# Optimization experiments

Hardware: AMD Instinct MI355X
Metric: run time of the kernel (lower is better)

## Reference

```python
import jax, jax.numpy as jnp
import numpy as np

N_NODES = 100000
IN_CH = 128
OUT_CH = 128
N_EDGES = 1700000


def setup_inputs() -> dict:
    key = jax.random.key(0)
    k_x, k_e, k_w = jax.random.split(key, 3)
    x = jax.random.normal(k_x, (N_NODES, IN_CH), dtype=jnp.float32)
    # edges: one self-loop per node (guarantees deg>=1 for every node),
    # remainder random
    loops = jnp.stack([jnp.arange(N_NODES, dtype=jnp.int64)] * 2)  # [2, N]
    rand = jax.random.randint(k_e, (2, N_EDGES - N_NODES), 0, N_NODES, dtype=jnp.int64)
    edge_index = jnp.concatenate([loops, rand], axis=1)  # [2, E]
    # glorot-uniform weight, zero bias (reset_parameters)
    limit = float(np.sqrt(6.0 / (IN_CH + OUT_CH)))
    weight = jax.random.uniform(k_w, (IN_CH, OUT_CH), dtype=jnp.float32,
                                minval=-limit, maxval=limit)
    bias = jnp.zeros((OUT_CH,), dtype=jnp.float32)
    return {"x": x, "edge_index": edge_index, "weight": weight, "bias": bias}


def reference(x, edge_index, weight, bias):
    row, col = edge_index[0], edge_index[1]
    # deg = bincount(row) over all N nodes
    deg = jax.ops.segment_sum(jnp.ones_like(row, dtype=jnp.float32), row,
                              num_segments=x.shape[0])
    deg_inv_sqrt = deg ** -0.5  # symmetric normalization
    norm = deg_inv_sqrt[row] * deg_inv_sqrt[col]  # [E]
    support = x @ weight  # [N, out]
    msgs = norm[:, None] * support[col]  # [E, out] gather + scale
    out = jax.ops.segment_sum(msgs, row, num_segments=x.shape[0])  # scatter-add
    return out + bias
```

## Files before the change

### kernel.cpp

```cpp
#include <hip/hip_runtime.h>
#include <hip/hip_bf16.h>


#define NBLK_B 512
#define BSHIFT 7
#define NPB    128

typedef __attribute__((ext_vector_type(8))) short bf16x8;
typedef __attribute__((ext_vector_type(4))) float f32x4;

__device__ __forceinline__ uint32_t f2bf_rne(float f) {
    uint32_t u = __float_as_uint(f);
    return (u + 0x7fffu + ((u >> 16) & 1u)) >> 16;
}
__device__ __forceinline__ float bf_lo(uint32_t u) { return __uint_as_float(u << 16); }
__device__ __forceinline__ float bf_hi(uint32_t u) { return __uint_as_float(u & 0xffff0000u); }

__device__ __forceinline__ bf16x8 pack8(float4 lo, float4 hi) {
    union { bf16x8 v; ushort u[8]; } r;
    r.u[0] = (ushort)f2bf_rne(lo.x);
    r.u[1] = (ushort)f2bf_rne(lo.y);
    r.u[2] = (ushort)f2bf_rne(lo.z);
    r.u[3] = (ushort)f2bf_rne(lo.w);
    r.u[4] = (ushort)f2bf_rne(hi.x);
    r.u[5] = (ushort)f2bf_rne(hi.y);
    r.u[6] = (ushort)f2bf_rne(hi.z);
    r.u[7] = (ushort)f2bf_rne(hi.w);
    return r.v;
}

__global__ void wconv_kernel(const float* __restrict__ W, ushort* __restrict__ Wt,
                             int* __restrict__ gcur, int nbuck) {
    int t = blockIdx.x * blockDim.x + threadIdx.x;
    int n = t >> 7, k = t & 127;
    Wt[n * 128 + k] = (ushort)f2bf_rne(W[k * 128 + n]);
    if (t < nbuck) gcur[t] = 0;
}

__global__ __launch_bounds__(256) void merged_kernel(
        const float* __restrict__ X, const ushort* __restrict__ Wt,
        uint32_t* __restrict__ S, int N,
        const int* __restrict__ row, const int* __restrict__ col,
        uint32_t* __restrict__ part, int* __restrict__ gcur,
        int E, int chunk, int nbuck, int cap, int GB) {
    __shared__ int h[1024];
    if ((int)blockIdx.x < GB) {
        const int wave = threadIdx.x >> 6;
        const int lane = threadIdx.x & 63;
        const int c16  = lane & 15;
        const int kg   = lane >> 4;
        const int row0 = blockIdx.x * 128 + wave * 32;

        int rA0 = row0 + c16;
        int rA1 = row0 + 16 + c16;
        if (rA0 >= N) rA0 = N - 1;
        if (rA1 >= N) rA1 = N - 1;

        f32x4 acc[2][8];
#pragma unroll
        for (int m = 0; m < 2; ++m)
#pragma unroll
            for (int cb = 0; cb < 8; ++cb) acc[m][cb] = (f32x4){0.f, 0.f, 0.f, 0.f};

        const float*  xa0 = X + (size_t)rA0 * 128 + kg * 8;
        const float*  xa1 = X + (size_t)rA1 * 128 + kg * 8;
        const ushort* wb  = Wt + kg * 8 + c16 * 128;

#pragma unroll
        for (int kk = 0; kk < 4; ++kk) {
            float4 a0lo = *(const float4*)(xa0 + kk * 32);
            float4 a0hi = *(const float4*)(xa0 + kk * 32 + 4);
            float4 a1lo = *(const float4*)(xa1 + kk * 32);
            float4 a1hi = *(const float4*)(xa1 + kk * 32 + 4);
            bf16x8 A0 = pack8(a0lo, a0hi);
            bf16x8 A1 = pack8(a1lo, a1hi);
#pragma unroll
            for (int cb = 0; cb < 8; ++cb) {
                bf16x8 B = *(const bf16x8*)(wb + (size_t)cb * 16 * 128 + kk * 32);
                acc[0][cb] = __builtin_amdgcn_mfma_f32_16x16x32_bf16(A0, B, acc[0][cb], 0, 0, 0);
                acc[1][cb] = __builtin_amdgcn_mfma_f32_16x16x32_bf16(A1, B, acc[1][cb], 0, 0, 0);
            }
        }
#pragma unroll
        for (int m = 0; m < 2; ++m) {
#pragma unroll
            for (int i = 0; i < 4; ++i) {
                int gr = row0 + m * 16 + kg * 4 + i;
                if (gr < N) {
#pragma unroll
                    for (int cb = 0; cb < 4; ++cb) {
                        uint32_t p = f2bf_rne(acc[m][cb][i]) |
                                     (f2bf_rne(acc[m][cb + 4][i]) << 16);
                        S[(size_t)gr * 64 + cb * 16 + c16] = p;
                    }
                }
            }
        }
    } else {
        const int blk = blockIdx.x - GB;
        const int t = threadIdx.x;
        for (int i = t; i < nbuck; i += 256) h[i] = 0;
        __syncthreads();
        int lo = blk * chunk, hi = min(E, lo + chunk);
        for (int e = lo + t; e < hi; e += 256) atomicAdd(&h[row[e] >> BSHIFT], 1);
        __syncthreads();
        for (int b = t; b < nbuck; b += 256) {
            int c = h[b];
            h[b] = (c > 0) ? atomicAdd(&gcur[b], c) : 0;
        }
        __syncthreads();
        for (int e = lo + t; e < hi; e += 256) {
            int r = row[e], c = col[e];
            int b = r >> BSHIFT;
            int pos = atomicAdd(&h[b], 1);
            if (pos < cap)
                part[(size_t)b * cap + pos] = ((uint32_t)(r & (NPB - 1)) << 17) | (uint32_t)c;
        }
    }
}

__global__ __launch_bounds__(256) void p3_build(const uint32_t* __restrict__ part,
                                                const int* __restrict__ gcur,
                                                int* __restrict__ rowstart,
                                                int* __restrict__ rowend,
                                                float* __restrict__ dis,
                                                int* __restrict__ csr,
                                                int N, int nbuck, int cap) {
    __shared__ int hist[NPB];
    __shared__ int lstart[NPB];
    __shared__ int sbuf[NPB];
    const int b = blockIdx.x, t = threadIdx.x;
    const int base = b * cap;
    int cb = gcur[b];
    if (cb > cap) cb = cap;

    if (t < NPB) hist[t] = 0;
    __syncthreads();
    for (int e = base + t; e < base + cb; e += 256)
        atomicAdd(&hist[part[e] >> 17], 1);
    __syncthreads();

    int v = (t < NPB) ? hist[t] : 0;
    if (t < NPB) sbuf[t] = v;
    __syncthreads();
#pragma unroll
    for (int o = 1; o < NPB; o <<= 1) {
        int u = 0;
        if (t < NPB && t >= o) u = sbuf[t - o];
        __syncthreads();
        if (t < NPB && t >= o) sbuf[t] += u;
        __syncthreads();
    }
    if (t < NPB) {
        int ex = sbuf[t] - v;
        lstart[t] = ex;
        int node = (b << BSHIFT) + t;
        if (node < N) {
            rowstart[node] = base + ex;
            rowend[node]   = base + ex + v;
            dis[node]      = rsqrtf((float)v);
        }
        hist[t] = ex;
    }
    __syncthreads();
    for (int e = base + t; e < base + cb; e += 256) {
        uint32_t p = part[e];
        int pos = base + atomicAdd(&hist[p >> 17], 1);
        csr[pos] = (int)(p & 0x1FFFFu);
    }
}

__global__ __launch_bounds__(256) void gather_kernel(const int* __restrict__ csr,
                                                     const int* __restrict__ rowstart,
                                                     const int* __restrict__ rowend,
                                                     const float* __restrict__ dis,
                                                     const uint4* __restrict__ sup,
                                                     const float* __restrict__ bias,
                                                     float* __restrict__ out, int N) {
    int wid  = (blockIdx.x * blockDim.x + threadIdx.x) >> 6;
    int lane = threadIdx.x & 63;
    if (wid >= N) return;
    const int grp = lane >> 4;
    const int li  = lane & 15;
    int begin = rowstart[wid];
    int end   = rowend[wid];
    int endm1 = end - 1;
    float dr  = dis[wid];

    float4 aL = make_float4(0.f, 0.f, 0.f, 0.f);
    float4 aH = make_float4(0.f, 0.f, 0.f, 0.f);

    for (int j = begin; j < end; j += 8) {
        int e0 = j + grp, e1 = j + 4 + grp;
        int c0 = csr[min(e0, endm1)];
        int c1 = csr[min(e1, endm1)];
        float n0 = (e0 < end) ? dr * dis[c0] : 0.f;
        float n1 = (e1 < end) ? dr * dis[c1] : 0.f;
        uint4 u0 = sup[(size_t)c0 * 16 + li];
        uint4 u1 = sup[(size_t)c1 * 16 + li];
        aL.x += n0 * bf_lo(u0.x) + n1 * bf_lo(u1.x);
        aL.y += n0 * bf_lo(u0.y) + n1 * bf_lo(u1.y);
        aL.z += n0 * bf_lo(u0.z) + n1 * bf_lo(u1.z);
        aL.w += n0 * bf_lo(u0.w) + n1 * bf_lo(u1.w);
        aH.x += n0 * bf_hi(u0.x) + n1 * bf_hi(u1.x);
        aH.y += n0 * bf_hi(u0.y) + n1 * bf_hi(u1.y);
        aH.z += n0 * bf_hi(u0.z) + n1 * bf_hi(u1.z);
        aH.w += n0 * bf_hi(u0.w) + n1 * bf_hi(u1.w);
    }

#pragma unroll
    for (int off = 16; off < 64; off <<= 1) {
        aL.x += __shfl_xor(aL.x, off);
        aL.y += __shfl_xor(aL.y, off);
        aL.z += __shfl_xor(aL.z, off);
        aL.w += __shfl_xor(aL.w, off);
        aH.x += __shfl_xor(aH.x, off);
        aH.y += __shfl_xor(aH.y, off);
        aH.z += __shfl_xor(aH.z, off);
        aH.w += __shfl_xor(aH.w, off);
    }

    if (grp == 0) {
        float4 bL = *(const float4*)(bias + li * 4);
        float4 bH = *(const float4*)(bias + 64 + li * 4);
        aL.x += bL.x; aL.y += bL.y; aL.z += bL.z; aL.w += bL.w;
        aH.x += bH.x; aH.y += bH.y; aH.z += bH.z; aH.w += bH.w;
        *(float4*)(out + (size_t)wid * 128 + li * 4)      = aL;
        *(float4*)(out + (size_t)wid * 128 + 64 + li * 4) = aH;
    }
}

#define SCAN_B 256
__global__ void scan_block_kernel(const int* __restrict__ in, int* __restrict__ outp,
                                  int* __restrict__ bsum, int M) {
    __shared__ int s[SCAN_B];
    int t = threadIdx.x;
    int g = blockIdx.x * SCAN_B + t;
    int v = (g < M) ? in[g] : 0;
    s[t] = v;
    __syncthreads();
#pragma unroll
    for (int off = 1; off < SCAN_B; off <<= 1) {
        int u = (t >= off) ? s[t - off] : 0;
        __syncthreads();
        s[t] += u;
        __syncthreads();
    }
    if (g < M) outp[g] = s[t] - v;
    if (t == SCAN_B - 1) bsum[blockIdx.x] = s[t];
}
__global__ void scan_bsum_kernel(int* __restrict__ bsum, int NB) {
    __shared__ int s[1024];
    int t = threadIdx.x;
    int v = (t < NB) ? bsum[t] : 0;
    s[t] = v;
    __syncthreads();
#pragma unroll
    for (int off = 1; off < 1024; off <<= 1) {
        int u = (t >= off) ? s[t - off] : 0;
        __syncthreads();
        s[t] += u;
        __syncthreads();
    }
    if (t < NB) bsum[t] = s[t] - v;
}
__global__ void scan_add_kernel(int* __restrict__ outp, const int* __restrict__ bsum, int M) {
    int g = blockIdx.x * blockDim.x + threadIdx.x;
    if (g < M) outp[g] += bsum[g >> 8];
}
#define GB_M 64
#define GB_KC 32
__global__ __launch_bounds__(256) void gemm_kernel(const float* __restrict__ X,
                                                   const float* __restrict__ W,
                                                   uint32_t* __restrict__ S, int N) {
    __shared__ float sXT[GB_KC][72];
    __shared__ float sW[GB_KC][128];
    const int t  = threadIdx.x;
    const int tx = t & 15;
    const int ty = t >> 4;
    const int bm = blockIdx.x * GB_M;

    float acc[4][8];
#pragma unroll
    for (int i = 0; i < 4; ++i)
#pragma unroll
        for (int j = 0; j < 8; ++j) acc[i][j] = 0.f;

    const int sr = t >> 2;
    const int sc = (t & 3) << 2;

    for (int k0 = 0; k0 < 128; k0 += GB_KC) {
#pragma unroll
        for (int h = 0; h < 2; ++h) {
            int kk = sc + h * 16;
            int gr = bm + sr;
            float4 v = make_float4(0.f, 0.f, 0.f, 0.f);
            if (gr < N) v = *(const float4*)(X + (size_t)gr * 128 + k0 + kk);
            sXT[kk + 0][sr] = v.x;
            sXT[kk + 1][sr] = v.y;
            sXT[kk + 2][sr] = v.z;
            sXT[kk + 3][sr] = v.w;
        }
#pragma unroll
        for (int h = 0; h < 4; ++h) {
            int idx = t + h * 256;
            int wk  = idx >> 5;
            int wo  = (idx & 31) << 2;
            *(float4*)&sW[wk][wo] = *(const float4*)(W + (size_t)(k0 + wk) * 128 + wo);
        }
        __syncthreads();
#pragma unroll
        for (int k = 0; k < GB_KC; ++k) {
            float4 a  = *(const float4*)&sXT[k][ty * 4];
            float4 b0 = *(const float4*)&sW[k][tx * 4];
            float4 b1 = *(const float4*)&sW[k][64 + tx * 4];
            float av[4] = {a.x, a.y, a.z, a.w};
            float bv[8] = {b0.x, b0.y, b0.z, b0.w, b1.x, b1.y, b1.z, b1.w};
#pragma unroll
            for (int i = 0; i < 4; ++i)
#pragma unroll
                for (int j = 0; j < 8; ++j) acc[i][j] += av[i] * bv[j];
        }
        __syncthreads();
    }
#pragma unroll
    for (int i = 0; i < 4; ++i) {
        int gr = bm + ty * 4 + i;
        if (gr < N) {
            uint4 q;
            q.x = f2bf_rne(acc[i][0]) | (f2bf_rne(acc[i][4]) << 16);
            q.y = f2bf_rne(acc[i][1]) | (f2bf_rne(acc[i][5]) << 16);
            q.z = f2bf_rne(acc[i][2]) | (f2bf_rne(acc[i][6]) << 16);
            q.w = f2bf_rne(acc[i][3]) | (f2bf_rne(acc[i][7]) << 16);
            *(uint4*)(S + (size_t)gr * 64 + tx * 4) = q;
        }
    }
}
__global__ void deg_i_kernel(const int* __restrict__ row, int* __restrict__ degi, int E) {
    int g = blockIdx.x * blockDim.x + threadIdx.x;
    if (g < E) atomicAdd(&degi[row[g]], 1);
}
__global__ void rsqrt_i_kernel(const int* __restrict__ degi, float* __restrict__ dis, int N) {
    int g = blockIdx.x * blockDim.x + threadIdx.x;
    if (g < N) dis[g] = rsqrtf((float)degi[g]);
}
__global__ void fill_kernel(const int* __restrict__ row, const int* __restrict__ col,
                            int* __restrict__ start, int* __restrict__ csr, int E) {
    int e = blockIdx.x * blockDim.x + threadIdx.x;
    if (e < E) {
        int pos = atomicAdd(&start[row[e]], 1);
        csr[pos] = col[e];
    }
}
__global__ void rowptr_from_start_kernel(const int* __restrict__ startv,
                                         int* __restrict__ rowptr, int N, int E) {
    int g = blockIdx.x * blockDim.x + threadIdx.x;
    if (g < N) rowptr[g] = startv[g];
    if (g == 0) rowptr[N] = E;
}

extern "C" void kernel_launch(void* const* d_in, const int* in_sizes, int n_in,
                              void* d_out, int out_size, void* d_ws, size_t ws_size,
                              hipStream_t stream) {
    const float* x    = (const float*)d_in[0];
    const int*   ei   = (const int*)d_in[1];
    const float* W    = (const float*)d_in[2];
    const float* bias = (const float*)d_in[3];
    float*       out  = (float*)d_out;

    const int N = in_sizes[0] / 128;
    const int E = in_sizes[1] / 2;
    const int* row = ei;
    const int* col = ei + E;

    const int nbuck = (N + NPB - 1) >> BSHIFT;
    int cap = (E + nbuck - 1) / nbuck;
    cap += cap / 4 + 64;
    cap = (cap + 63) & ~63;
    const int chunkB = (E + NBLK_B - 1) / NBLK_B;
    const int GB = (N + 127) / 128;

    auto al = [](size_t v) { return (v + 511) & ~(size_t)511; };
    size_t o_gcur = 0;
    size_t o_rs   = al(o_gcur + (size_t)nbuck * 4);
    size_t o_re   = al(o_rs + (size_t)N * 4);
    size_t o_dis  = al(o_re + (size_t)N * 4);
    size_t o_csr  = al(o_dis + (size_t)N * 4);
    size_t o_part = al(o_csr + (size_t)nbuck * cap * 4);
    size_t o_wt   = al(o_part + (size_t)nbuck * cap * 4);
    size_t o_sup  = al(o_wt + 128 * 128 * 2);
    size_t need   = o_sup + (size_t)N * 256;

    char* ws = (char*)d_ws;

    if (ws_size >= need && nbuck <= 1024 && N <= (1 << 17)) {
        int*      gcur = (int*)(ws + o_gcur);
        int*      rs   = (int*)(ws + o_rs);
        int*      re   = (int*)(ws + o_re);
        float*    dis  = (float*)(ws + o_dis);
        int*      csr  = (int*)(ws + o_csr);
        uint32_t* part = (uint32_t*)(ws + o_part);
        ushort*   wt   = (ushort*)(ws + o_wt);
        uint4*    sup  = (uint4*)(ws + o_sup);

        wconv_kernel<<<64, 256, 0, stream>>>(W, wt, gcur, nbuck);
        merged_kernel<<<GB + NBLK_B, 256, 0, stream>>>(
            x, wt, (uint32_t*)sup, N, row, col, part, gcur,
            E, chunkB, nbuck, cap, GB);
        p3_build<<<nbuck, 256, 0, stream>>>(part, gcur, rs, re, dis, csr,
                                            N, nbuck, cap);
        long long gthreads = (long long)N * 64;
        gather_kernel<<<(int)((gthreads + 255) / 256), 256, 0, stream>>>(
            csr, rs, re, dis, sup, bias, out, N);
    } else {
        size_t f_degi   = 0;
        size_t f_dis    = al(f_degi + (size_t)N * 4);
        size_t f_start  = al(f_dis + (size_t)N * 4);
        size_t f_rowptr = al(f_start + (size_t)N * 4);
        size_t f_bsum   = al(f_rowptr + ((size_t)N + 1) * 4);
        size_t f_csr    = al(f_bsum + 4096 * 4);
        size_t f_sup    = al(f_csr + (size_t)E * 4);

        int*      degi   = (int*)(ws + f_degi);
        float*    dis    = (float*)(ws + f_dis);
        int*      startv = (int*)(ws + f_start);
        int*      rowptr = (int*)(ws + f_rowptr);
        int*      bsum   = (int*)(ws + f_bsum);
        int*      csr    = (int*)(ws + f_csr);
        uint4*    sup    = (uint4*)(ws + f_sup);
        const int NBn = (N + SCAN_B - 1) / SCAN_B;

        hipMemsetAsync(degi, 0, (size_t)N * 4, stream);
        gemm_kernel<<<(N + GB_M - 1) / GB_M, 256, 0, stream>>>(x, W, (uint32_t*)sup, N);
        deg_i_kernel<<<(E + 255) / 256, 256, 0, stream>>>(row, degi, E);
        scan_block_kernel<<<NBn, SCAN_B, 0, stream>>>(degi, startv, bsum, N);
        scan_bsum_kernel<<<1, 1024, 0, stream>>>(bsum, NBn);
        scan_add_kernel<<<NBn, SCAN_B, 0, stream>>>(startv, bsum, N);
        rowptr_from_start_kernel<<<NBn, SCAN_B, 0, stream>>>(startv, rowptr, N, E);
        rsqrt_i_kernel<<<NBn, SCAN_B, 0, stream>>>(degi, dis, N);
        fill_kernel<<<(E + 255) / 256, 256, 0, stream>>>(row, col, startv, csr, E);
        long long gthreads = (long long)N * 64;
        gather_kernel<<<(int)((gthreads + 255) / 256), 256, 0, stream>>>(
            csr, rowptr, rowptr + 1, dis, sup, bias, out, N);
    }
}
```

Measured before the change: 146.3 us.

## Stage bucket partition and CSR build in shared memory for coalesced writes

```diff
diff --git a/kernel.cpp b/kernel.cpp
--- a/kernel.cpp
+++ b/kernel.cpp
@@ -2,9 +2,11 @@
 #include <hip/hip_bf16.h>
 
 
-#define NBLK_B 512
-#define BSHIFT 7
-#define NPB    128
+#define NBLK_B  512
+#define BSHIFT  8
+#define NPB     256
+#define REC_CAP 3456
+#define CAPMAX  5632
 
 typedef __attribute__((ext_vector_type(8))) short bf16x8;
 typedef __attribute__((ext_vector_type(4))) float f32x4;
@@ -43,7 +45,7 @@
         const int* __restrict__ row, const int* __restrict__ col,
         uint32_t* __restrict__ part, int* __restrict__ gcur,
         int E, int chunk, int nbuck, int cap, int GB) {
-    __shared__ int h[1024];
+    __shared__ __align__(16) char smem[26880];
     if ((int)blockIdx.x < GB) {
         const int wave = threadIdx.x >> 6;
         const int lane = threadIdx.x & 63;
@@ -97,38 +99,72 @@
             }
         }
     } else {
+        uint32_t* rec  = (uint32_t*)smem;
+        ushort*   rbk  = (ushort*)(smem + 13824);
+        int*      hist = (int*)(smem + 20736);
+        int*      lst  = (int*)(smem + 22784);
+        int*      resv = (int*)(smem + 24832);
         const int blk = blockIdx.x - GB;
         const int t = threadIdx.x;
-        for (int i = t; i < nbuck; i += 256) h[i] = 0;
-        __syncthreads();
         int lo = blk * chunk, hi = min(E, lo + chunk);
-        for (int e = lo + t; e < hi; e += 256) atomicAdd(&h[row[e] >> BSHIFT], 1);
+        int cnt = hi - lo;
+
+        for (int i = t; i < 512; i += 256) hist[i] = 0;
+        __syncthreads();
+        for (int i = t; i < cnt; i += 256)
+            atomicAdd(&hist[row[lo + i] >> BSHIFT], 1);
+        __syncthreads();
+        int a0 = hist[2 * t], a1 = hist[2 * t + 1];
+        int v2 = a0 + a1;
+        resv[t] = v2;
+        __syncthreads();
+#pragma unroll
+        for (int o = 1; o < 256; o <<= 1) {
+            int u = (t >= o) ? resv[t - o] : 0;
+            __syncthreads();
+            resv[t] += u;
+            __syncthreads();
+        }
+        int ex = resv[t] - v2;
+        lst[2 * t]     = ex;
+        lst[2 * t + 1] = ex + a0;
         __syncthreads();
         for (int b = t; b < nbuck; b += 256) {
-            int c = h[b];
-            h[b] = (c > 0) ? atomicAdd(&gcur[b], c) : 0;
-        }
-        __syncthreads();
-        for (int e = lo + t; e < hi; e += 256) {
-            int r = row[e], c = col[e];
+            int c = hist[b];
+            resv[b] = (c > 0) ? atomicAdd(&gcur[b], c) : 0;
+        }
+        __syncthreads();
+        for (int i = t; i < 512; i += 256) hist[i] = lst[i];
+        __syncthreads();
+        for (int i = t; i < cnt; i += 256) {
+            int r = row[lo + i], c = col[lo + i];
             int b = r >> BSHIFT;
-            int pos = atomicAdd(&h[b], 1);
-            if (pos < cap)
-                part[(size_t)b * cap + pos] = ((uint32_t)(r & (NPB - 1)) << 17) | (uint32_t)c;
-        }
-    }
-}
-
-__global__ __launch_bounds__(256) void p3_build(const uint32_t* __restrict__ part,
+            int p = atomicAdd(&hist[b], 1);
+            rec[p] = ((uint32_t)(r & (NPB - 1)) << 17) | (uint32_t)c;
+            rbk[p] = (ushort)b;
+        }
+        __syncthreads();
+        for (int i = t; i < cnt; i += 256) {
+            int b = rbk[i];
+            int off = resv[b] + (i - lst[b]);
+            if (off < cap)
+                part[(size_t)b * cap + off] = rec[i];
+        }
+    }
+}
+
+__global__ __launch_bounds__(512) void p3_build(const uint32_t* __restrict__ part,
                                                 const int* __restrict__ gcur,
                                                 int* __restrict__ rowstart,
                                                 int* __restrict__ rowend,
                                                 float* __restrict__ dis,
                                                 int* __restrict__ csr,
                                                 int N, int nbuck, int cap) {
+    __shared__ uint32_t recl[CAPMAX];
+    __shared__ int csrl[CAPMAX];
     __shared__ int hist[NPB];
-    __shared__ int lstart[NPB];
-    __shared__ int sbuf[NPB];
+    __shared__ int lst[NPB];
+    __shared__ int s[NPB];
     const int b = blockIdx.x, t = threadIdx.x;
     const int base = b * cap;
     int cb = gcur[b];
@@ -136,24 +172,27 @@
 
     if (t < NPB) hist[t] = 0;
     __syncthreads();
-    for (int e = base + t; e < base + cb; e += 256)
-        atomicAdd(&hist[part[e] >> 17], 1);
-    __syncthreads();
-
-    int v = (t < NPB) ? hist[t] : 0;
-    if (t < NPB) sbuf[t] = v;
+    for (int i = t; i < cb; i += 512) {
+        uint32_t p = part[base + i];
+        recl[i] = p;
+        atomicAdd(&hist[p >> 17], 1);
+    }
+    __syncthreads();
+
+    int v = 0;
+    if (t < NPB) { v = hist[t]; s[t] = v; }
     __syncthreads();
 #pragma unroll
     for (int o = 1; o < NPB; o <<= 1) {
         int u = 0;
-        if (t < NPB && t >= o) u = sbuf[t - o];
-        __syncthreads();
-        if (t < NPB && t >= o) sbuf[t] += u;
+        if (t < NPB && t >= o) u = s[t - o];
+        __syncthreads();
+        if (t < NPB && t >= o) s[t] += u;
         __syncthreads();
     }
     if (t < NPB) {
-        int ex = sbuf[t] - v;
-        lstart[t] = ex;
+        int ex = s[t] - v;
+        lst[t] = ex;
         int node = (b << BSHIFT) + t;
         if (node < N) {
             rowstart[node] = base + ex;
@@ -163,11 +202,14 @@
         hist[t] = ex;
     }
     __syncthreads();
-    for (int e = base + t; e < base + cb; e += 256) {
-        uint32_t p = part[e];
-        int pos = base + atomicAdd(&hist[p >> 17], 1);
-        csr[pos] = (int)(p & 0x1FFFFu);
-    }
+    for (int i = t; i < cb; i += 512) {
+        uint32_t p = recl[i];
+        int q = atomicAdd(&hist[p >> 17], 1);
+        csrl[q] = (int)(p & 0x1FFFFu);
+    }
+    __syncthreads();
+    for (int i = t; i < cb; i += 512)
+        csr[base + i] = csrl[i];
 }
 
 __global__ __launch_bounds__(256) void gather_kernel(const int* __restrict__ csr,
@@ -375,7 +417,7 @@
 
     const int nbuck = (N + NPB - 1) >> BSHIFT;
     int cap = (E + nbuck - 1) / nbuck;
-    cap += cap / 4 + 64;
+    cap += cap / 4 + 128;
     cap = (cap + 63) & ~63;
     const int chunkB = (E + NBLK_B - 1) / NBLK_B;
     const int GB = (N + 127) / 128;
@@ -393,7 +435,8 @@
 
     char* ws = (char*)d_ws;
 
-    if (ws_size >= need && nbuck <= 1024 && N <= (1 << 17)) {
+    if (ws_size >= need && nbuck <= 512 && N <= (1 << 17) &&
+        cap <= CAPMAX && chunkB <= REC_CAP) {
         int*      gcur = (int*)(ws + o_gcur);
         int*      rs   = (int*)(ws + o_rs);
         int*      re   = (int*)(ws + o_re);
@@ -407,7 +450,7 @@
         merged_kernel<<<GB + NBLK_B, 256, 0, stream>>>(
             x, wt, (uint32_t*)sup, N, row, col, part, gcur,
             E, chunkB, nbuck, cap, GB);
-        p3_build<<<nbuck, 256, 0, stream>>>(part, gcur, rs, re, dis, csr,
+        p3_build<<<nbuck, 512, 0, stream>>>(part, gcur, rs, re, dis, csr,
                                             N, nbuck, cap);
         long long gthreads = (long long)N * 64;
         gather_kernel<<<(int)((gthreads + 255) / 256), 256, 0, stream>>>(
```

Result: faster. 133.8 us (-8.5%).
